# Performance work log

Hardware: AMD Instinct MI355X
Metric: run time of the kernel (lower is better)

Reference implementation:

```python
import jax, jax.numpy as jnp
import numpy as np


def conv1x1(x, w, b):
    # x: [B,C,H,W], w: [O,C], b: [O] -> [B,O,H,W]
    return jnp.einsum('bchw,oc->bohw', x, w) + b[None, :, None, None]


def maxpool2x2(x):
    B, C, H, W = x.shape
    return x.reshape(B, C, H // 2, 2, W // 2, 2).max(axis=(3, 5))


def setup_inputs() -> dict:
    key = jax.random.key(0)
    ks = jax.random.split(key, 10)
    C = 256
    x = jax.random.normal(ks[0], (16, C, 64, 64), dtype=jnp.float32)
    s = lambda fan_in: 1.0 / np.sqrt(fan_in)
    w_theta = jax.random.normal(ks[1], (C // 8, C), dtype=jnp.float32) * s(C)
    b_theta = jax.random.normal(ks[2], (C // 8,), dtype=jnp.float32) * 0.01
    w_phi = jax.random.normal(ks[3], (C // 8, C), dtype=jnp.float32) * s(C)
    b_phi = jax.random.normal(ks[4], (C // 8,), dtype=jnp.float32) * 0.01
    w_g = jax.random.normal(ks[5], (C // 2, C), dtype=jnp.float32) * s(C)
    b_g = jax.random.normal(ks[6], (C // 2,), dtype=jnp.float32) * 0.01
    w_attn = jax.random.normal(ks[7], (C, C // 2), dtype=jnp.float32) * s(C // 2)
    b_attn = jax.random.normal(ks[8], (C,), dtype=jnp.float32) * 0.01
    sigma = jnp.full((1,), 0.5, dtype=jnp.float32)
    return {"x": x, "w_theta": w_theta, "b_theta": b_theta,
            "w_phi": w_phi, "b_phi": b_phi, "w_g": w_g, "b_g": b_g,
            "w_attn": w_attn, "b_attn": b_attn, "sigma": sigma}


def reference(x, w_theta, b_theta, w_phi, b_phi, w_g, b_g, w_attn, b_attn, sigma):
    B, C, W, H = x.shape
    N = W * H
    N4 = N // 4
    # Q: [B, N, C/8]
    theta = conv1x1(x, w_theta, b_theta).reshape(B, C // 8, N).transpose(0, 2, 1)
    # K: [B, C/8, N/4] (2x2 maxpool downsample)
    phi = maxpool2x2(conv1x1(x, w_phi, b_phi)).reshape(B, C // 8, N4)
    # attention: [B, N, N/4]
    attn = jax.nn.softmax(jnp.einsum('bnc,bcm->bnm', theta, phi), axis=-1)
    # V: [B, N/4, C/2]
    g = maxpool2x2(conv1x1(x, w_g, b_g)).reshape(B, C // 2, N4).transpose(0, 2, 1)
    attn_g = jnp.einsum('bnm,bmc->bnc', attn, g).transpose(0, 2, 1).reshape(B, C // 2, W, H)
    attn_g = conv1x1(attn_g, w_attn, b_attn)
    return x + sigma[0] * attn_g
```

## Files before the change

### kernel.cpp

```cpp
#include <hip/hip_runtime.h>
#include <math.h>

#define BATCH 16
#define CIN   256
#define NPIX  4096
#define NP4   1024
#define DQK   32
#define DV    128
#define KT    64
#define QW    32
#define QT    128

typedef __attribute__((ext_vector_type(8)))  short short8v;
typedef __attribute__((ext_vector_type(16))) float f32x16;

#define ZERO16 {0.f,0.f,0.f,0.f,0.f,0.f,0.f,0.f,0.f,0.f,0.f,0.f,0.f,0.f,0.f,0.f}

__device__ __forceinline__ unsigned short f2bf(float f) {
    unsigned u = __float_as_uint(f);
    u += 0x7FFFu + ((u >> 16) & 1u);
    return (unsigned short)(u >> 16);
}

__device__ __forceinline__ unsigned cvtpk(float a, float b) {
    unsigned r;
    asm("v_cvt_pk_bf16_f32 %0, %1, %2" : "=v"(r) : "v"(a), "v"(b));
    return r;
}

__device__ __forceinline__ void gload_lds16(const void* g, void* l) {
    __builtin_amdgcn_global_load_lds(
        (const __attribute__((address_space(1))) unsigned int*)g,
        (__attribute__((address_space(3))) unsigned int*)l, 16, 0, 0);
}

#define VMCNT0_BARRIER() do { \
    asm volatile("s_waitcnt vmcnt(0)" ::: "memory"); \
    __syncthreads(); \
} while (0)

__global__ void wcvt_k(const float* __restrict__ wt, const float* __restrict__ wp,
                       const float* __restrict__ wg, const float* __restrict__ wa,
                       unsigned short* __restrict__ wqkv, unsigned short* __restrict__ wab)
{
    int i = blockIdx.x * 256 + threadIdx.x;
    if (i < 192 * 256) {
        int row = i >> 8, c = i & 255;
        float v = row < 32 ? wt[row * 256 + c]
                : row < 64 ? wp[(row - 32) * 256 + c]
                           : wg[(row - 64) * 256 + c];
        wqkv[i] = f2bf(v);
    } else {
        int j = i - 192 * 256;
        if (j < 256 * DV) wab[j] = f2bf(wa[j]);
    }
}

__global__ __launch_bounds__(256, 2) void conv_qkv_k(
    const float* __restrict__ x, const unsigned short* __restrict__ wqkv,
    const float* __restrict__ b_theta, const float* __restrict__ b_phi,
    const float* __restrict__ b_g, unsigned short* __restrict__ Qg,
    unsigned short* __restrict__ Kg, unsigned short* __restrict__ Vg)
{
    __shared__ __align__(16) union {
        unsigned short xs[2][2][128][8];
        float pool[2][160][32];
    } u;

    const int b    = blockIdx.y;
    const int tile = blockIdx.x;
    const int pixb = tile * 128;
    const int t    = threadIdx.x;
    const int wv   = t >> 6, l = t & 63, h = l >> 5, q31 = l & 31;
    const int sp   = t & 127, skb = t >> 7;

    const float* xb = x + (size_t)b * CIN * NPIX + pixb + sp;

    f32x16 acc[6];
#pragma unroll
    for (int i = 0; i < 6; ++i) acc[i] = ZERO16;

    float xa[8], xbr[8];
#pragma unroll
    for (int j = 0; j < 8; ++j) xa[j] = xb[(size_t)(skb * 8 + j) * NPIX];
    {
        unsigned pk[4];
#pragma unroll
        for (int jj = 0; jj < 4; ++jj) pk[jj] = cvtpk(xa[2*jj], xa[2*jj+1]);
        *(uint4*)&u.xs[0][skb][sp][0] = *(uint4*)pk;
    }
#pragma unroll
    for (int j = 0; j < 8; ++j) xbr[j] = xb[(size_t)(16 + skb * 8 + j) * NPIX];
    __syncthreads();

    for (int ks = 0; ks < 16; ks += 2) {
        if (ks < 14) {
            const float* xn = xb + (size_t)((ks + 2) * 16 + skb * 8) * NPIX;
#pragma unroll
            for (int j = 0; j < 8; ++j) xa[j] = xn[(size_t)j * NPIX];
        }
        {
            short8v bf = *(const short8v*)&u.xs[0][h][wv * 32 + q31][0];
#pragma unroll
            for (int rb = 0; rb < 6; ++rb) {
                short8v af = *(const short8v*)&wqkv[(size_t)(rb * 32 + q31) * 256 + ks * 16 + h * 8];
                acc[rb] = __builtin_amdgcn_mfma_f32_32x32x16_bf16(af, bf, acc[rb], 0, 0, 0);
            }
        }
        {
            unsigned pk[4];
#pragma unroll
            for (int jj = 0; jj < 4; ++jj) pk[jj] = cvtpk(xbr[2*jj], xbr[2*jj+1]);
            *(uint4*)&u.xs[1][skb][sp][0] = *(uint4*)pk;
        }
        __syncthreads();

        if (ks < 14) {
            const float* xn = xb + (size_t)((ks + 3) * 16 + skb * 8) * NPIX;
#pragma unroll
            for (int j = 0; j < 8; ++j) xbr[j] = xn[(size_t)j * NPIX];
        }
        {
            short8v bf = *(const short8v*)&u.xs[1][h][wv * 32 + q31][0];
#pragma unroll
            for (int rb = 0; rb < 6; ++rb) {
                short8v af = *(const short8v*)&wqkv[(size_t)(rb * 32 + q31) * 256 + (ks + 1) * 16 + h * 8];
                acc[rb] = __builtin_amdgcn_mfma_f32_32x32x16_bf16(af, bf, acc[rb], 0, 0, 0);
            }
        }
        if (ks < 14) {
            unsigned pk[4];
#pragma unroll
            for (int jj = 0; jj < 4; ++jj) pk[jj] = cvtpk(xa[2*jj], xa[2*jj+1]);
            *(uint4*)&u.xs[0][skb][sp][0] = *(uint4*)pk;
        }
        __syncthreads();
    }

    {
        int pix = pixb + wv * 32 + q31;
        unsigned short* qout = &Qg[((size_t)b * NPIX + pix) * DQK];
#pragma unroll
        for (int m = 0; m < 4; ++m) {
            unsigned pk2[2];
            float v0 = acc[0][m*4+0] + b_theta[4*h + 8*m + 0];
            float v1 = acc[0][m*4+1] + b_theta[4*h + 8*m + 1];
            float v2 = acc[0][m*4+2] + b_theta[4*h + 8*m + 2];
            float v3 = acc[0][m*4+3] + b_theta[4*h + 8*m + 3];
            pk2[0] = cvtpk(v0, v1);
            pk2[1] = cvtpk(v2, v3);
            *(uint2*)&qout[8*m + 4*h] = *(uint2*)pk2;
        }
    }

#pragma unroll
    for (int rb = 1; rb < 6; ++rb) {
#pragma unroll
        for (int r = 0; r < 16; ++r) {
            float v  = acc[rb][r];
            float o  = __shfl_xor(v, 1);
            float mx = fmaxf(v, o);
            if ((q31 & 1) == 0) {
                int row = (r & 3) + 8 * (r >> 2) + 4 * h;
                u.pool[wv >> 1][(rb - 1) * 32 + row][(wv & 1) * 16 + (q31 >> 1)] = mx;
            }
        }
    }
    __syncthreads();

    {
        int wx = t & 31;
        int pp = tile * 32 + wx;
#pragma unroll
        for (int i = 0; i < 20; ++i) {
            int ch = (t >> 5) * 20 + i;
            float v = fmaxf(u.pool[0][ch][wx], u.pool[1][ch][wx]);
            if (ch < 32) {
                v += b_phi[ch];
                Kg[(((size_t)b * 4 + (ch >> 3)) * NP4 + pp) * 8 + (ch & 7)] = f2bf(v);
            } else {
                int c = ch - 32;
                v += b_g[c];
                Vg[((size_t)b * 128 + (pp >> 3)) * (DV * 8) + (size_t)c * 8 + (pp & 7)] = f2bf(v);
            }
        }
    }
}

__global__ __launch_bounds__(256, 2) void flash_k(
    const unsigned short* __restrict__ Qg, const unsigned short* __restrict__ Kg,
    const unsigned short* __restrict__ Vg, const unsigned short* __restrict__ wab,
    const float* __restrict__ b_attn, const float* __restrict__ sigma,
    const float* __restrict__ x, float* __restrict__ out)
{
    __shared__ __align__(16) union {
        struct {
            unsigned short ks[2][4 * KT * 8];
            unsigned short vs[2][8 * DV * 8];
        } s;
        unsigned short os[4][16 * QW * 8];
    } u;

    const int b   = blockIdx.y;
    const int t   = threadIdx.x;
    const int wv  = t >> 6;
    const int l   = t & 63;
    const int h   = l >> 5;
    const int q31 = l & 31;
    const int p0  = blockIdx.x * QT + wv * QW;

    const size_t kbase = (size_t)b * 4 * NP4 * 8;
    const size_t vbase = (size_t)b * 128 * DV * 8;

    auto STAGE = [&](int bu, int kt) {
#pragma unroll
        for (int j = 0; j < 5; ++j) {
            int cid = wv * 5 + j;
            if (cid < 4) {
                gload_lds16(&Kg[kbase + ((size_t)cid * NP4 + kt * KT + l) * 8],
                            &u.s.ks[bu][cid * 512]);
            } else {
                int c2 = cid - 4;
                gload_lds16(&Vg[vbase + (size_t)kt * 8192 + c2 * 512 + l * 8],
                            &u.s.vs[bu][c2 * 512]);
            }
        }
    };

    short8v qf0 = *(const short8v*)&Qg[((size_t)b * NPIX + p0 + q31) * DQK + h * 8];
    short8v qf1 = *(const short8v*)&Qg[((size_t)b * NPIX + p0 + q31) * DQK + 16 + h * 8];

    f32x16 o0 = ZERO16, o1 = ZERO16, o2 = ZERO16, o3 = ZERO16;
    float m = -3.0e38f, lsum = 0.f;

    STAGE(0, 0);
    VMCNT0_BARRIER();
    int cur = 0;

    for (int kt = 0; kt < NP4 / KT; ++kt) {
        if (kt < NP4 / KT - 1) STAGE(cur ^ 1, kt + 1);

        f32x16 s0 = ZERO16, s1 = ZERO16;
        {
            short8v kf;
            kf = *(const short8v*)&u.s.ks[cur][((0 + h) * KT + 0 + q31) * 8];
            s0 = __builtin_amdgcn_mfma_f32_32x32x16_bf16(kf, qf0, s0, 0, 0, 0);
            kf = *(const short8v*)&u.s.ks[cur][((2 + h) * KT + 0 + q31) * 8];
            s0 = __builtin_amdgcn_mfma_f32_32x32x16_bf16(kf, qf1, s0, 0, 0, 0);
            kf = *(const short8v*)&u.s.ks[cur][((0 + h) * KT + 32 + q31) * 8];
            s1 = __builtin_amdgcn_mfma_f32_32x32x16_bf16(kf, qf0, s1, 0, 0, 0);
            kf = *(const short8v*)&u.s.ks[cur][((2 + h) * KT + 32 + q31) * 8];
            s1 = __builtin_amdgcn_mfma_f32_32x32x16_bf16(kf, qf1, s1, 0, 0, 0);
        }

        float mx = s0[0];
#pragma unroll
        for (int r = 1; r < 16; ++r) mx = fmaxf(mx, s0[r]);
#pragma unroll
        for (int r = 0; r < 16; ++r) mx = fmaxf(mx, s1[r]);
        mx = fmaxf(mx, __shfl_xor(mx, 32));

        bool nskip = !__all(mx <= m + 8.0f);
        if (nskip) {
            float mnew = fmaxf(m, mx);
            float scale = __expf(m - mnew);
            m = mnew;
            lsum *= scale;
#pragma unroll
            for (int r = 0; r < 16; ++r) {
                float sc = __shfl(scale, (r & 3) + 8 * (r >> 2) + 4 * h);
                o0[r] *= sc; o1[r] *= sc; o2[r] *= sc; o3[r] *= sc;
            }
        }

        float rs = 0.f;
#pragma unroll
        for (int r = 0; r < 16; ++r) { s0[r] = __expf(s0[r] - m); rs += s0[r]; }
#pragma unroll
        for (int r = 0; r < 16; ++r) { s1[r] = __expf(s1[r] - m); rs += s1[r]; }
        rs += __shfl_xor(rs, 32);
        lsum += rs;

        unsigned ca[8], cb[8], da[8], db[8];
#pragma unroll
        for (int j = 0; j < 8; ++j) {
            ca[j] = cvtpk(s0[2*j], s0[2*j+1]);
            cb[j] = cvtpk(s1[2*j], s1[2*j+1]);
        }
#pragma unroll
        for (int j = 0; j < 8; ++j) {
            da[j] = (unsigned)__shfl_xor((int)ca[j], 32);
            db[j] = (unsigned)__shfl_xor((int)cb[j], 32);
        }
        union { unsigned uu[4]; short8v v; } pa[4];
#pragma unroll
        for (int ksl = 0; ksl < 2; ++ksl) {
            pa[ksl].uu[0]     = h ? da[4*ksl+2] : ca[4*ksl+0];
            pa[ksl].uu[1]     = h ? da[4*ksl+3] : ca[4*ksl+1];
            pa[ksl].uu[2]     = h ? ca[4*ksl+2] : da[4*ksl+0];
            pa[ksl].uu[3]     = h ? ca[4*ksl+3] : da[4*ksl+1];
            pa[2+ksl].uu[0]   = h ? db[4*ksl+2] : cb[4*ksl+0];
            pa[2+ksl].uu[1]   = h ? db[4*ksl+3] : cb[4*ksl+1];
            pa[2+ksl].uu[2]   = h ? cb[4*ksl+2] : db[4*ksl+0];
            pa[2+ksl].uu[3]   = h ? cb[4*ksl+3] : db[4*ksl+1];
        }

#pragma unroll
        for (int ks16 = 0; ks16 < 4; ++ks16) {
            const unsigned short* vrow = &u.s.vs[cur][((ks16 * 2 + h) * DV) * 8];
            o0 = __builtin_amdgcn_mfma_f32_32x32x16_bf16(pa[ks16].v,
                     *(const short8v*)&vrow[(0  + q31) * 8], o0, 0, 0, 0);
            o1 = __builtin_amdgcn_mfma_f32_32x32x16_bf16(pa[ks16].v,
                     *(const short8v*)&vrow[(32 + q31) * 8], o1, 0, 0, 0);
            o2 = __builtin_amdgcn_mfma_f32_32x32x16_bf16(pa[ks16].v,
                     *(const short8v*)&vrow[(64 + q31) * 8], o2, 0, 0, 0);
            o3 = __builtin_amdgcn_mfma_f32_32x32x16_bf16(pa[ks16].v,
                     *(const short8v*)&vrow[(96 + q31) * 8], o3, 0, 0, 0);
        }

        VMCNT0_BARRIER();
        cur ^= 1;
    }

    float rinv = 1.0f / lsum;
    unsigned short* osw = u.os[wv];
#pragma unroll
    for (int r = 0; r < 16; ++r) {
        float rn = __shfl(rinv, (r & 3) + 8 * (r >> 2) + 4 * h);
        int q = (r & 3) + 8 * (r >> 2) + 4 * h;
        osw[((0 * 4 + (q31 >> 3)) * QW + q) * 8 + (l & 7)] = f2bf(o0[r] * rn);
        osw[((1 * 4 + (q31 >> 3)) * QW + q) * 8 + (l & 7)] = f2bf(o1[r] * rn);
        osw[((2 * 4 + (q31 >> 3)) * QW + q) * 8 + (l & 7)] = f2bf(o2[r] * rn);
        osw[((3 * 4 + (q31 >> 3)) * QW + q) * 8 + (l & 7)] = f2bf(o3[r] * rn);
    }

    const float sg = sigma[0];
    for (int cht = 0; cht < 8; ++cht) {
        f32x16 e = ZERO16;
#pragma unroll
        for (int ks16 = 0; ks16 < 8; ++ks16) {
            short8v wf = *(const short8v*)&wab[(size_t)(cht * 32 + q31) * DV + ks16 * 16 + h * 8];
            short8v of = *(const short8v*)&osw[((ks16 * 2 + h) * QW + q31) * 8];
            e = __builtin_amdgcn_mfma_f32_32x32x16_bf16(wf, of, e, 0, 0, 0);
        }
#pragma unroll
        for (int r = 0; r < 16; ++r) {
            int ch = cht * 32 + (r & 3) + 8 * (r >> 2) + 4 * h;
            size_t idx = ((size_t)b * 256 + ch) * NPIX + p0 + q31;
            out[idx] = fmaf(sg, e[r] + b_attn[ch], x[idx]);
        }
    }
}

extern "C" void kernel_launch(void* const* d_in, const int* in_sizes, int n_in,
                              void* d_out, int out_size, void* d_ws, size_t ws_size,
                              hipStream_t stream) {
    const float* x       = (const float*)d_in[0];
    const float* w_theta = (const float*)d_in[1];
    const float* b_theta = (const float*)d_in[2];
    const float* w_phi   = (const float*)d_in[3];
    const float* b_phi   = (const float*)d_in[4];
    const float* w_g     = (const float*)d_in[5];
    const float* b_g     = (const float*)d_in[6];
    const float* w_attn  = (const float*)d_in[7];
    const float* b_attn  = (const float*)d_in[8];
    const float* sigma   = (const float*)d_in[9];
    float* out = (float*)d_out;

    unsigned short* Qg   = (unsigned short*)d_ws;
    unsigned short* Kg   = Qg + (size_t)BATCH * NPIX * DQK;
    unsigned short* Vg   = Kg + (size_t)BATCH * 4 * NP4 * 8;
    unsigned short* wab  = Vg + (size_t)BATCH * 128 * DV * 8;
    unsigned short* wqkv = wab + (size_t)256 * DV;

    wcvt_k    <<<dim3((192 * 256 + 256 * DV + 255) / 256), 256, 0, stream>>>(
        w_theta, w_phi, w_g, w_attn, wqkv, wab);
    conv_qkv_k<<<dim3(NPIX / 128, BATCH), 256, 0, stream>>>(
        x, wqkv, b_theta, b_phi, b_g, Qg, Kg, Vg);
    flash_k   <<<dim3(NPIX / QT, BATCH), 256, 0, stream>>>(
        Qg, Kg, Vg, wab, b_attn, sigma, x, out);
}
```

Measured before the change: 99.49 us.

## Split KV range across two wave groups in flash kernel and use exp2 softmax

The flash kernel now runs 512 threads per block. Two groups of four waves each process half of the key/value range for the same 128 queries, and their partial max and sum are merged through shared memory before the output projection. Q is prescaled by log2(e) in the conv kernel so the softmax can use exp2f, and the max and sum reductions are restructured as trees. This aims to halve the serial KV loop per wave and raise occupancy. In exchange it doubles LDS staging, adds block-wide syncs, and sums two bf16-rounded partial outputs in the projection.

```diff
diff --git a/kernel.cpp b/kernel.cpp
--- a/kernel.cpp
+++ b/kernel.cpp
@@ -15,6 +15,7 @@
 typedef __attribute__((ext_vector_type(16))) float f32x16;
 
 #define ZERO16 {0.f,0.f,0.f,0.f,0.f,0.f,0.f,0.f,0.f,0.f,0.f,0.f,0.f,0.f,0.f,0.f}
+#define LOG2E 1.44269504088896340736f
 
 __device__ __forceinline__ unsigned short f2bf(float f) {
     unsigned u = __float_as_uint(f);
@@ -143,10 +144,10 @@
 #pragma unroll
         for (int m = 0; m < 4; ++m) {
             unsigned pk2[2];
-            float v0 = acc[0][m*4+0] + b_theta[4*h + 8*m + 0];
-            float v1 = acc[0][m*4+1] + b_theta[4*h + 8*m + 1];
-            float v2 = acc[0][m*4+2] + b_theta[4*h + 8*m + 2];
-            float v3 = acc[0][m*4+3] + b_theta[4*h + 8*m + 3];
+            float v0 = (acc[0][m*4+0] + b_theta[4*h + 8*m + 0]) * LOG2E;
+            float v1 = (acc[0][m*4+1] + b_theta[4*h + 8*m + 1]) * LOG2E;
+            float v2 = (acc[0][m*4+2] + b_theta[4*h + 8*m + 2]) * LOG2E;
+            float v3 = (acc[0][m*4+3] + b_theta[4*h + 8*m + 3]) * LOG2E;
             pk2[0] = cvtpk(v0, v1);
             pk2[1] = cvtpk(v2, v3);
             *(uint2*)&qout[8*m + 4*h] = *(uint2*)pk2;
@@ -187,7 +188,7 @@
     }
 }
 
-__global__ __launch_bounds__(256, 2) void flash_k(
+__global__ __launch_bounds__(512, 4) void flash_k(
     const unsigned short* __restrict__ Qg, const unsigned short* __restrict__ Kg,
     const unsigned short* __restrict__ Vg, const unsigned short* __restrict__ wab,
     const float* __restrict__ b_attn, const float* __restrict__ sigma,
@@ -195,34 +196,42 @@
 {
     __shared__ __align__(16) union {
         struct {
-            unsigned short ks[2][4 * KT * 8];
-            unsigned short vs[2][8 * DV * 8];
+            unsigned short ks[2][2][4 * KT * 8];
+            unsigned short vs[2][2][8 * DV * 8];
         } s;
-        unsigned short os[4][16 * QW * 8];
+        struct {
+            unsigned short os[2][4][16 * QW * 8];
+            float ml[2][2][4][32];
+        } e;
     } u;
 
-    const int b   = blockIdx.y;
-    const int t   = threadIdx.x;
-    const int wv  = t >> 6;
-    const int l   = t & 63;
-    const int h   = l >> 5;
-    const int q31 = l & 31;
-    const int p0  = blockIdx.x * QT + wv * QW;
+    const int b    = blockIdx.y;
+    const int t    = threadIdx.x;
+    const int wv   = t >> 6;
+    const int sub  = wv & 3;
+    const int half = wv >> 2;
+    const int l    = t & 63;
+    const int h    = l >> 5;
+    const int q31  = l & 31;
+    const int p0   = blockIdx.x * QT + sub * QW;
 
     const size_t kbase = (size_t)b * 4 * NP4 * 8;
     const size_t vbase = (size_t)b * 128 * DV * 8;
 
-    auto STAGE = [&](int bu, int kt) {
+    auto STAGE = [&](int bu, int step) {
 #pragma unroll
         for (int j = 0; j < 5; ++j) {
             int cid = wv * 5 + j;
-            if (cid < 4) {
-                gload_lds16(&Kg[kbase + ((size_t)cid * NP4 + kt * KT + l) * 8],
-                            &u.s.ks[bu][cid * 512]);
+            int hf  = cid < 20 ? 0 : 1;
+            int c   = cid - hf * 20;
+            int kt  = hf ? 8 + step : step;
+            if (c < 4) {
+                gload_lds16(&Kg[kbase + ((size_t)c * NP4 + kt * KT + l) * 8],
+                            &u.s.ks[bu][hf][c * 512]);
             } else {
-                int c2 = cid - 4;
+                int c2 = c - 4;
                 gload_lds16(&Vg[vbase + (size_t)kt * 8192 + c2 * 512 + l * 8],
-                            &u.s.vs[bu][c2 * 512]);
+                            &u.s.vs[bu][hf][c2 * 512]);
             }
         }
     };
@@ -237,33 +246,38 @@
     VMCNT0_BARRIER();
     int cur = 0;
 
-    for (int kt = 0; kt < NP4 / KT; ++kt) {
-        if (kt < NP4 / KT - 1) STAGE(cur ^ 1, kt + 1);
+    for (int i = 0; i < 8; ++i) {
+        if (i < 7) STAGE(cur ^ 1, i + 1);
+
+        const unsigned short* kbuf = u.s.ks[cur][half];
+        const unsigned short* vbuf = u.s.vs[cur][half];
 
         f32x16 s0 = ZERO16, s1 = ZERO16;
         {
             short8v kf;
-            kf = *(const short8v*)&u.s.ks[cur][((0 + h) * KT + 0 + q31) * 8];
+            kf = *(const short8v*)&kbuf[((0 + h) * KT + 0 + q31) * 8];
             s0 = __builtin_amdgcn_mfma_f32_32x32x16_bf16(kf, qf0, s0, 0, 0, 0);
-            kf = *(const short8v*)&u.s.ks[cur][((2 + h) * KT + 0 + q31) * 8];
+            kf = *(const short8v*)&kbuf[((2 + h) * KT + 0 + q31) * 8];
             s0 = __builtin_amdgcn_mfma_f32_32x32x16_bf16(kf, qf1, s0, 0, 0, 0);
-            kf = *(const short8v*)&u.s.ks[cur][((0 + h) * KT + 32 + q31) * 8];
+            kf = *(const short8v*)&kbuf[((0 + h) * KT + 32 + q31) * 8];
             s1 = __builtin_amdgcn_mfma_f32_32x32x16_bf16(kf, qf0, s1, 0, 0, 0);
-            kf = *(const short8v*)&u.s.ks[cur][((2 + h) * KT + 32 + q31) * 8];
+            kf = *(const short8v*)&kbuf[((2 + h) * KT + 32 + q31) * 8];
             s1 = __builtin_amdgcn_mfma_f32_32x32x16_bf16(kf, qf1, s1, 0, 0, 0);
         }
 
-        float mx = s0[0];
-#pragma unroll
-        for (int r = 1; r < 16; ++r) mx = fmaxf(mx, s0[r]);
-#pragma unroll
-        for (int r = 0; r < 16; ++r) mx = fmaxf(mx, s1[r]);
-        mx = fmaxf(mx, __shfl_xor(mx, 32));
-
-        bool nskip = !__all(mx <= m + 8.0f);
+        float tm[16];
+#pragma unroll
+        for (int r = 0; r < 16; ++r) tm[r] = fmaxf(s0[r], s1[r]);
+#pragma unroll
+        for (int d = 8; d >= 1; d >>= 1)
+#pragma unroll
+            for (int r = 0; r < d; ++r) tm[r] = fmaxf(tm[r], tm[r + d]);
+        float mx = fmaxf(tm[0], __shfl_xor(tm[0], 32));
+
+        bool nskip = !__all(mx <= m + 11.5f);
         if (nskip) {
             float mnew = fmaxf(m, mx);
-            float scale = __expf(m - mnew);
+            float scale = exp2f(m - mnew);
             m = mnew;
             lsum *= scale;
 #pragma unroll
@@ -273,13 +287,18 @@
             }
         }
 
-        float rs = 0.f;
-#pragma unroll
-        for (int r = 0; r < 16; ++r) { s0[r] = __expf(s0[r] - m); rs += s0[r]; }
-#pragma unroll
-        for (int r = 0; r < 16; ++r) { s1[r] = __expf(s1[r] - m); rs += s1[r]; }
-        rs += __shfl_xor(rs, 32);
-        lsum += rs;
+        float ts[16];
+#pragma unroll
+        for (int r = 0; r < 16; ++r) {
+            s0[r] = exp2f(s0[r] - m);
+            s1[r] = exp2f(s1[r] - m);
+            ts[r] = s0[r] + s1[r];
+        }
+#pragma unroll
+        for (int d = 8; d >= 1; d >>= 1)
+#pragma unroll
+            for (int r = 0; r < d; ++r) ts[r] += ts[r + d];
+        lsum += ts[0] + __shfl_xor(ts[0], 32);
 
         unsigned ca[8], cb[8], da[8], db[8];
 #pragma unroll
@@ -307,7 +326,7 @@
 
 #pragma unroll
         for (int ks16 = 0; ks16 < 4; ++ks16) {
-            const unsigned short* vrow = &u.s.vs[cur][((ks16 * 2 + h) * DV) * 8];
+            const unsigned short* vrow = &vbuf[((ks16 * 2 + h) * DV) * 8];
             o0 = __builtin_amdgcn_mfma_f32_32x32x16_bf16(pa[ks16].v,
                      *(const short8v*)&vrow[(0  + q31) * 8], o0, 0, 0, 0);
             o1 = __builtin_amdgcn_mfma_f32_32x32x16_bf16(pa[ks16].v,
@@ -322,26 +341,42 @@
         cur ^= 1;
     }
 
-    float rinv = 1.0f / lsum;
-    unsigned short* osw = u.os[wv];
+    if (h == 0) {
+        u.e.ml[0][half][sub][q31] = m;
+        u.e.ml[1][half][sub][q31] = lsum;
+    }
+    __syncthreads();
+    float m1 = u.e.ml[0][0][sub][q31], l1 = u.e.ml[1][0][sub][q31];
+    float m2 = u.e.ml[0][1][sub][q31], l2 = u.e.ml[1][1][sub][q31];
+    float m12 = fmaxf(m1, m2);
+    float l12 = l1 * exp2f(m1 - m12) + l2 * exp2f(m2 - m12);
+    float rinv = exp2f(m - m12) / l12;
+
+    unsigned short* osw = u.e.os[half][sub];
 #pragma unroll
     for (int r = 0; r < 16; ++r) {
-        float rn = __shfl(rinv, (r & 3) + 8 * (r >> 2) + 4 * h);
         int q = (r & 3) + 8 * (r >> 2) + 4 * h;
+        float rn = __shfl(rinv, q);
         osw[((0 * 4 + (q31 >> 3)) * QW + q) * 8 + (l & 7)] = f2bf(o0[r] * rn);
         osw[((1 * 4 + (q31 >> 3)) * QW + q) * 8 + (l & 7)] = f2bf(o1[r] * rn);
         osw[((2 * 4 + (q31 >> 3)) * QW + q) * 8 + (l & 7)] = f2bf(o2[r] * rn);
         osw[((3 * 4 + (q31 >> 3)) * QW + q) * 8 + (l & 7)] = f2bf(o3[r] * rn);
     }
+    __syncthreads();
 
     const float sg = sigma[0];
-    for (int cht = 0; cht < 8; ++cht) {
+    for (int cc = 0; cc < 4; ++cc) {
+        int cht = half * 4 + cc;
         f32x16 e = ZERO16;
 #pragma unroll
-        for (int ks16 = 0; ks16 < 8; ++ks16) {
-            short8v wf = *(const short8v*)&wab[(size_t)(cht * 32 + q31) * DV + ks16 * 16 + h * 8];
-            short8v of = *(const short8v*)&osw[((ks16 * 2 + h) * QW + q31) * 8];
-            e = __builtin_amdgcn_mfma_f32_32x32x16_bf16(wf, of, e, 0, 0, 0);
+        for (int hf2 = 0; hf2 < 2; ++hf2) {
+            const unsigned short* osr = u.e.os[hf2][sub];
+#pragma unroll
+            for (int ks16 = 0; ks16 < 8; ++ks16) {
+                short8v wf = *(const short8v*)&wab[(size_t)(cht * 32 + q31) * DV + ks16 * 16 + h * 8];
+                short8v of = *(const short8v*)&osr[((ks16 * 2 + h) * QW + q31) * 8];
+                e = __builtin_amdgcn_mfma_f32_32x32x16_bf16(wf, of, e, 0, 0, 0);
+            }
         }
 #pragma unroll
         for (int r = 0; r < 16; ++r) {
@@ -377,6 +412,6 @@
         w_theta, w_phi, w_g, w_attn, wqkv, wab);
     conv_qkv_k<<<dim3(NPIX / 128, BATCH), 256, 0, stream>>>(
         x, wqkv, b_theta, b_phi, b_g, Qg, Kg, Vg);
-    flash_k   <<<dim3(NPIX / QT, BATCH), 256, 0, stream>>>(
+    flash_k   <<<dim3(NPIX / QT, BATCH), 512, 0, stream>>>(
         Qg, Kg, Vg, wab, b_attn, sigma, x, out);
 }
```

Result: slower. 179.1 us (+80.0%).

## Load K/V directly into registers, use exp2 softmax and permlane swaps

Applied to the files above, without the earlier changes.

Drops the LDS double-buffered staging of K and V tiles. Each wave now loads its MFMA fragments straight from global memory into registers, with software prefetch of the next tile interleaved with compute, which removes the per-tile barriers. Q is pre-scaled by log2(e) so the softmax can use exp2f, the lazy-rescale threshold is raised to match the log2 scale, and max/sum reductions become tree-shaped. The P-operand lane exchange uses v_permlane32_swap instead of shuffles. The trade-off is higher register pressure, and every wave redundantly fetches the same K/V from L2 instead of sharing it through LDS.

```diff
diff --git a/kernel.cpp b/kernel.cpp
--- a/kernel.cpp
+++ b/kernel.cpp
@@ -15,6 +15,7 @@
 typedef __attribute__((ext_vector_type(16))) float f32x16;
 
 #define ZERO16 {0.f,0.f,0.f,0.f,0.f,0.f,0.f,0.f,0.f,0.f,0.f,0.f,0.f,0.f,0.f,0.f}
+#define LOG2E 1.44269504088896340736f
 
 __device__ __forceinline__ unsigned short f2bf(float f) {
     unsigned u = __float_as_uint(f);
@@ -28,16 +29,11 @@
     return r;
 }
 
-__device__ __forceinline__ void gload_lds16(const void* g, void* l) {
-    __builtin_amdgcn_global_load_lds(
-        (const __attribute__((address_space(1))) unsigned int*)g,
-        (__attribute__((address_space(3))) unsigned int*)l, 16, 0, 0);
-}
-
-#define VMCNT0_BARRIER() do { \
-    asm volatile("s_waitcnt vmcnt(0)" ::: "memory"); \
-    __syncthreads(); \
-} while (0)
+__device__ __forceinline__ short8v ldg8(const unsigned short* p) {
+    return *(const short8v*)p;
+}
+
+#define PLSWAP(a, b) asm("v_permlane32_swap_b32 %0, %1" : "+v"(a), "+v"(b))
 
 __global__ void wcvt_k(const float* __restrict__ wt, const float* __restrict__ wp,
                        const float* __restrict__ wg, const float* __restrict__ wa,
@@ -143,10 +139,10 @@
 #pragma unroll
         for (int m = 0; m < 4; ++m) {
             unsigned pk2[2];
-            float v0 = acc[0][m*4+0] + b_theta[4*h + 8*m + 0];
-            float v1 = acc[0][m*4+1] + b_theta[4*h + 8*m + 1];
-            float v2 = acc[0][m*4+2] + b_theta[4*h + 8*m + 2];
-            float v3 = acc[0][m*4+3] + b_theta[4*h + 8*m + 3];
+            float v0 = (acc[0][m*4+0] + b_theta[4*h + 8*m + 0]) * LOG2E;
+            float v1 = (acc[0][m*4+1] + b_theta[4*h + 8*m + 1]) * LOG2E;
+            float v2 = (acc[0][m*4+2] + b_theta[4*h + 8*m + 2]) * LOG2E;
+            float v3 = (acc[0][m*4+3] + b_theta[4*h + 8*m + 3]) * LOG2E;
             pk2[0] = cvtpk(v0, v1);
             pk2[1] = cvtpk(v2, v3);
             *(uint2*)&qout[8*m + 4*h] = *(uint2*)pk2;
@@ -193,13 +189,7 @@
     const float* __restrict__ b_attn, const float* __restrict__ sigma,
     const float* __restrict__ x, float* __restrict__ out)
 {
-    __shared__ __align__(16) union {
-        struct {
-            unsigned short ks[2][4 * KT * 8];
-            unsigned short vs[2][8 * DV * 8];
-        } s;
-        unsigned short os[4][16 * QW * 8];
-    } u;
+    __shared__ __align__(16) unsigned short os[4][16 * QW * 8];
 
     const int b   = blockIdx.y;
     const int t   = threadIdx.x;
@@ -209,61 +199,52 @@
     const int q31 = l & 31;
     const int p0  = blockIdx.x * QT + wv * QW;
 
-    const size_t kbase = (size_t)b * 4 * NP4 * 8;
-    const size_t vbase = (size_t)b * 128 * DV * 8;
-
-    auto STAGE = [&](int bu, int kt) {
-#pragma unroll
-        for (int j = 0; j < 5; ++j) {
-            int cid = wv * 5 + j;
-            if (cid < 4) {
-                gload_lds16(&Kg[kbase + ((size_t)cid * NP4 + kt * KT + l) * 8],
-                            &u.s.ks[bu][cid * 512]);
-            } else {
-                int c2 = cid - 4;
-                gload_lds16(&Vg[vbase + (size_t)kt * 8192 + c2 * 512 + l * 8],
-                            &u.s.vs[bu][c2 * 512]);
-            }
-        }
-    };
-
-    short8v qf0 = *(const short8v*)&Qg[((size_t)b * NPIX + p0 + q31) * DQK + h * 8];
-    short8v qf1 = *(const short8v*)&Qg[((size_t)b * NPIX + p0 + q31) * DQK + 16 + h * 8];
+    const unsigned short* Kp = Kg + (size_t)b * 4 * NP4 * 8 + ((size_t)h * NP4 + q31) * 8;
+    const unsigned short* Vp = Vg + (size_t)b * 128 * DV * 8 + h * 1024 + q31 * 8;
+
+    short8v qf0 = ldg8(&Qg[((size_t)b * NPIX + p0 + q31) * DQK + h * 8]);
+    short8v qf1 = ldg8(&Qg[((size_t)b * NPIX + p0 + q31) * DQK + 16 + h * 8]);
 
     f32x16 o0 = ZERO16, o1 = ZERO16, o2 = ZERO16, o3 = ZERO16;
     float m = -3.0e38f, lsum = 0.f;
 
-    STAGE(0, 0);
-    VMCNT0_BARRIER();
-    int cur = 0;
-
-    for (int kt = 0; kt < NP4 / KT; ++kt) {
-        if (kt < NP4 / KT - 1) STAGE(cur ^ 1, kt + 1);
-
+    short8v kfA[4], kfB[4], vg[16];
+#pragma unroll
+    for (int i = 0; i < 4; ++i)
+        kfA[i] = ldg8(Kp + (i >> 1) * (2 * NP4 * 8) + (i & 1) * 256);
+#pragma unroll
+    for (int g = 0; g < 4; ++g)
+#pragma unroll
+        for (int cc = 0; cc < 4; ++cc)
+            vg[g * 4 + cc] = ldg8(Vp + g * 2048 + cc * 256);
+
+    auto tile = [&](int kt, short8v (&kfc)[4], short8v (&kfn)[4], bool pref) {
         f32x16 s0 = ZERO16, s1 = ZERO16;
-        {
-            short8v kf;
-            kf = *(const short8v*)&u.s.ks[cur][((0 + h) * KT + 0 + q31) * 8];
-            s0 = __builtin_amdgcn_mfma_f32_32x32x16_bf16(kf, qf0, s0, 0, 0, 0);
-            kf = *(const short8v*)&u.s.ks[cur][((2 + h) * KT + 0 + q31) * 8];
-            s0 = __builtin_amdgcn_mfma_f32_32x32x16_bf16(kf, qf1, s0, 0, 0, 0);
-            kf = *(const short8v*)&u.s.ks[cur][((0 + h) * KT + 32 + q31) * 8];
-            s1 = __builtin_amdgcn_mfma_f32_32x32x16_bf16(kf, qf0, s1, 0, 0, 0);
-            kf = *(const short8v*)&u.s.ks[cur][((2 + h) * KT + 32 + q31) * 8];
-            s1 = __builtin_amdgcn_mfma_f32_32x32x16_bf16(kf, qf1, s1, 0, 0, 0);
-        }
-
-        float mx = s0[0];
-#pragma unroll
-        for (int r = 1; r < 16; ++r) mx = fmaxf(mx, s0[r]);
-#pragma unroll
-        for (int r = 0; r < 16; ++r) mx = fmaxf(mx, s1[r]);
-        mx = fmaxf(mx, __shfl_xor(mx, 32));
-
-        bool nskip = !__all(mx <= m + 8.0f);
+        s0 = __builtin_amdgcn_mfma_f32_32x32x16_bf16(kfc[0], qf0, s0, 0, 0, 0);
+        s0 = __builtin_amdgcn_mfma_f32_32x32x16_bf16(kfc[2], qf1, s0, 0, 0, 0);
+        s1 = __builtin_amdgcn_mfma_f32_32x32x16_bf16(kfc[1], qf0, s1, 0, 0, 0);
+        s1 = __builtin_amdgcn_mfma_f32_32x32x16_bf16(kfc[3], qf1, s1, 0, 0, 0);
+
+        if (pref) {
+            const unsigned short* kp1 = Kp + (size_t)(kt + 1) * 512;
+#pragma unroll
+            for (int i = 0; i < 4; ++i)
+                kfn[i] = ldg8(kp1 + (i >> 1) * (2 * NP4 * 8) + (i & 1) * 256);
+        }
+
+        float tm[16];
+#pragma unroll
+        for (int r = 0; r < 16; ++r) tm[r] = fmaxf(s0[r], s1[r]);
+#pragma unroll
+        for (int d = 8; d >= 1; d >>= 1)
+#pragma unroll
+            for (int r = 0; r < d; ++r) tm[r] = fmaxf(tm[r], tm[r + d]);
+        float mx = fmaxf(tm[0], __shfl_xor(tm[0], 32));
+
+        bool nskip = !__all(mx <= m + 11.5f);
         if (nskip) {
             float mnew = fmaxf(m, mx);
-            float scale = __expf(m - mnew);
+            float scale = exp2f(m - mnew);
             m = mnew;
             lsum *= scale;
 #pragma unroll
@@ -273,61 +254,62 @@
             }
         }
 
-        float rs = 0.f;
-#pragma unroll
-        for (int r = 0; r < 16; ++r) { s0[r] = __expf(s0[r] - m); rs += s0[r]; }
-#pragma unroll
-        for (int r = 0; r < 16; ++r) { s1[r] = __expf(s1[r] - m); rs += s1[r]; }
-        rs += __shfl_xor(rs, 32);
-        lsum += rs;
-
-        unsigned ca[8], cb[8], da[8], db[8];
+        float ts[16];
+#pragma unroll
+        for (int r = 0; r < 16; ++r) {
+            s0[r] = exp2f(s0[r] - m);
+            s1[r] = exp2f(s1[r] - m);
+            ts[r] = s0[r] + s1[r];
+        }
+#pragma unroll
+        for (int d = 8; d >= 1; d >>= 1)
+#pragma unroll
+            for (int r = 0; r < d; ++r) ts[r] += ts[r + d];
+        lsum += ts[0] + __shfl_xor(ts[0], 32);
+
+        unsigned ca[8], cb[8];
 #pragma unroll
         for (int j = 0; j < 8; ++j) {
             ca[j] = cvtpk(s0[2*j], s0[2*j+1]);
             cb[j] = cvtpk(s1[2*j], s1[2*j+1]);
         }
-#pragma unroll
-        for (int j = 0; j < 8; ++j) {
-            da[j] = (unsigned)__shfl_xor((int)ca[j], 32);
-            db[j] = (unsigned)__shfl_xor((int)cb[j], 32);
-        }
+        PLSWAP(ca[0], ca[2]); PLSWAP(ca[1], ca[3]);
+        PLSWAP(ca[4], ca[6]); PLSWAP(ca[5], ca[7]);
+        PLSWAP(cb[0], cb[2]); PLSWAP(cb[1], cb[3]);
+        PLSWAP(cb[4], cb[6]); PLSWAP(cb[5], cb[7]);
         union { unsigned uu[4]; short8v v; } pa[4];
 #pragma unroll
-        for (int ksl = 0; ksl < 2; ++ksl) {
-            pa[ksl].uu[0]     = h ? da[4*ksl+2] : ca[4*ksl+0];
-            pa[ksl].uu[1]     = h ? da[4*ksl+3] : ca[4*ksl+1];
-            pa[ksl].uu[2]     = h ? ca[4*ksl+2] : da[4*ksl+0];
-            pa[ksl].uu[3]     = h ? ca[4*ksl+3] : da[4*ksl+1];
-            pa[2+ksl].uu[0]   = h ? db[4*ksl+2] : cb[4*ksl+0];
-            pa[2+ksl].uu[1]   = h ? db[4*ksl+3] : cb[4*ksl+1];
-            pa[2+ksl].uu[2]   = h ? cb[4*ksl+2] : db[4*ksl+0];
-            pa[2+ksl].uu[3]   = h ? cb[4*ksl+3] : db[4*ksl+1];
-        }
-
-#pragma unroll
-        for (int ks16 = 0; ks16 < 4; ++ks16) {
-            const unsigned short* vrow = &u.s.vs[cur][((ks16 * 2 + h) * DV) * 8];
-            o0 = __builtin_amdgcn_mfma_f32_32x32x16_bf16(pa[ks16].v,
-                     *(const short8v*)&vrow[(0  + q31) * 8], o0, 0, 0, 0);
-            o1 = __builtin_amdgcn_mfma_f32_32x32x16_bf16(pa[ks16].v,
-                     *(const short8v*)&vrow[(32 + q31) * 8], o1, 0, 0, 0);
-            o2 = __builtin_amdgcn_mfma_f32_32x32x16_bf16(pa[ks16].v,
-                     *(const short8v*)&vrow[(64 + q31) * 8], o2, 0, 0, 0);
-            o3 = __builtin_amdgcn_mfma_f32_32x32x16_bf16(pa[ks16].v,
-                     *(const short8v*)&vrow[(96 + q31) * 8], o3, 0, 0, 0);
-        }
-
-        VMCNT0_BARRIER();
-        cur ^= 1;
+        for (int j = 0; j < 4; ++j) {
+            pa[0].uu[j] = ca[j];     pa[1].uu[j] = ca[4 + j];
+            pa[2].uu[j] = cb[j];     pa[3].uu[j] = cb[4 + j];
+        }
+
+        const unsigned short* vp1 = Vp + (size_t)(kt + 1) * 8192;
+#pragma unroll
+        for (int g = 0; g < 4; ++g) {
+            o0 = __builtin_amdgcn_mfma_f32_32x32x16_bf16(pa[g].v, vg[g*4+0], o0, 0, 0, 0);
+            o1 = __builtin_amdgcn_mfma_f32_32x32x16_bf16(pa[g].v, vg[g*4+1], o1, 0, 0, 0);
+            o2 = __builtin_amdgcn_mfma_f32_32x32x16_bf16(pa[g].v, vg[g*4+2], o2, 0, 0, 0);
+            o3 = __builtin_amdgcn_mfma_f32_32x32x16_bf16(pa[g].v, vg[g*4+3], o3, 0, 0, 0);
+            if (pref) {
+#pragma unroll
+                for (int cc = 0; cc < 4; ++cc)
+                    vg[g*4+cc] = ldg8(vp1 + g * 2048 + cc * 256);
+            }
+        }
+    };
+
+    for (int kt = 0; kt < 16; kt += 2) {
+        tile(kt,     kfA, kfB, true);
+        tile(kt + 1, kfB, kfA, kt + 1 < 15);
     }
 
     float rinv = 1.0f / lsum;
-    unsigned short* osw = u.os[wv];
+    unsigned short* osw = os[wv];
 #pragma unroll
     for (int r = 0; r < 16; ++r) {
-        float rn = __shfl(rinv, (r & 3) + 8 * (r >> 2) + 4 * h);
         int q = (r & 3) + 8 * (r >> 2) + 4 * h;
+        float rn = __shfl(rinv, q);
         osw[((0 * 4 + (q31 >> 3)) * QW + q) * 8 + (l & 7)] = f2bf(o0[r] * rn);
         osw[((1 * 4 + (q31 >> 3)) * QW + q) * 8 + (l & 7)] = f2bf(o1[r] * rn);
         osw[((2 * 4 + (q31 >> 3)) * QW + q) * 8 + (l & 7)] = f2bf(o2[r] * rn);
@@ -339,7 +321,7 @@
         f32x16 e = ZERO16;
 #pragma unroll
         for (int ks16 = 0; ks16 < 8; ++ks16) {
-            short8v wf = *(const short8v*)&wab[(size_t)(cht * 32 + q31) * DV + ks16 * 16 + h * 8];
+            short8v wf = ldg8(&wab[(size_t)(cht * 32 + q31) * DV + ks16 * 16 + h * 8]);
             short8v of = *(const short8v*)&osw[((ks16 * 2 + h) * QW + q31) * 8];
             e = __builtin_amdgcn_mfma_f32_32x32x16_bf16(wf, of, e, 0, 0, 0);
         }
```

Result: slower. 104.7 us (+5.3%).
